# Kernel optimization log

Hardware: AMD Instinct MI355X
Metric: run time of the kernel (lower is better)

## Reference

```python
import jax, jax.numpy as jnp
import numpy as np

B, C_IN, H, W = 8, 112, 16, 16
D = 128            # patch_embed_dim
N_BANK = 200000
CHUNK = 1024       # query_chunk_size
NN_K = 3
TOPK_RATIO = 0.03  # reduction = 'topk_mean'


def setup_inputs() -> dict:
    key = jax.random.key(0)
    k1, k2, k3 = jax.random.split(key, 3)
    feature_map = jax.random.normal(k1, (B, C_IN, H, W), dtype=jnp.float32)
    proj_w = jax.random.normal(k2, (D, C_IN), dtype=jnp.float32) * 0.05
    memory_bank = jax.random.normal(k3, (N_BANK, D), dtype=jnp.float32)
    return {"feature_map": feature_map, "proj_w": proj_w, "memory_bank": memory_bank}


def _l2norm(x, axis=-1, eps=1e-12):
    return x / jnp.maximum(jnp.linalg.norm(x, axis=axis, keepdims=True), eps)


def reference(feature_map, proj_w, memory_bank):
    b, c, h, w = feature_map.shape
    patches = h * w
    # patch embeddings: NHWC flatten -> linear proj (no bias) -> L2 normalize
    emb = feature_map.transpose(0, 2, 3, 1).reshape(-1, c)        # [Q, C_in]
    emb = _l2norm(emb @ proj_w.T)                                  # [Q, D]
    bank = _l2norm(memory_bank)                                    # [N, D]
    bank_t = bank.T                                                # [D, N]

    q_total = emb.shape[0]
    n_chunks = q_total // CHUNK if q_total % CHUNK == 0 else -(-q_total // CHUNK)
    pad = n_chunks * CHUNK - q_total
    emb_p = jnp.pad(emb, ((0, pad), (0, 0)))
    chunks = emb_p.reshape(n_chunks, CHUNK, -1)

    def chunk_fn(q):                                               # q: [CHUNK, D]
        sims = q @ bank_t                                          # [CHUNK, N]
        best_sim, _ = jax.lax.top_k(sims, NN_K)                    # [CHUNK, k]
        dist = jnp.sqrt(jnp.maximum(2.0 - 2.0 * best_sim, 0.0))
        return dist.mean(axis=1)                                   # [CHUNK]

    patch_d = jax.lax.map(chunk_fn, chunks).reshape(-1)[:q_total]
    patch_d = patch_d.reshape(b, patches)                          # [B, P]

    # topk_mean reduction over patches
    k = min(patches, max(1, int(np.ceil(patches * TOPK_RATIO))))
    top_vals, _ = jax.lax.top_k(patch_d, k)
    return top_vals.mean(axis=1)                                   # [B]
```

## Files before the change

### kernel.cpp

```cpp
#include <hip/hip_runtime.h>
#include <stdint.h>

#define N_BANK 200000
#define N_PAD  201600
#define NQ     2048
#define DIMD   128
#define C_IN   112
#define NCHUNK 63
#define CHUNK_COLS 3200
#define STEP_COLS 64
#define NSTEP  50
#define NCE    126
#define NC3    378

typedef short v8s __attribute__((ext_vector_type(8)));
typedef float v4f __attribute__((ext_vector_type(4)));

typedef const __attribute__((address_space(1))) uint32_t* gp1_t;
typedef __attribute__((address_space(3))) uint32_t* lp3_t;

__device__ __forceinline__ void async16(const void* g, void* l) {
  __builtin_amdgcn_global_load_lds((gp1_t)g, (lp3_t)l, 16, 0, 0);
}

__device__ __forceinline__ unsigned short f2bf(float f) {
  uint32_t u = __float_as_uint(f);
  u += 0x7fff + ((u >> 16) & 1);
  return (unsigned short)(u >> 16);
}

__device__ __forceinline__ void insert3(float& m1, float& m2, float& m3, float v) {
  m3 = __builtin_amdgcn_fmed3f(m2, m3, v);
  m2 = __builtin_amdgcn_fmed3f(m1, m2, v);
  m1 = fmaxf(m1, v);
}

__global__ void emb_kernel(const float* __restrict__ fm, const float* __restrict__ pw,
                           unsigned short* __restrict__ embB) {
  int q = blockIdx.x;
  int b = q >> 8, p = q & 255;
  int tid = threadIdx.x;
  __shared__ float x[C_IN];
  __shared__ float wsum[2];
  if (tid < C_IN) x[tid] = fm[(b * C_IN + tid) * 256 + p];
  __syncthreads();
  const float* row = pw + tid * C_IN;
  float dot = 0.f;
#pragma unroll
  for (int c = 0; c < C_IN; ++c) dot = fmaf(x[c], row[c], dot);
  float s = dot * dot;
#pragma unroll
  for (int off = 32; off; off >>= 1) s += __shfl_xor(s, off);
  int lane = tid & 63, wv = tid >> 6;
  if (lane == 0) wsum[wv] = s;
  __syncthreads();
  float ss = wsum[0] + wsum[1];
  float scale = 1.f / fmaxf(sqrtf(ss), 1e-12f);
  int j = tid >> 3, pos = tid & 7;
  int sw = j ^ (q & 15);
  embB[q * DIMD + sw * 8 + pos] = f2bf(dot * scale);
}

__global__ void bank_kernel(const float* __restrict__ bank, unsigned short* __restrict__ bankB) {
  int tid = threadIdx.x;
  int wv = tid >> 6, lane = tid & 63;
  int r = blockIdx.x * 4 + wv;
  if (r >= N_PAD) return;
  uint32_t* out = (uint32_t*)bankB;
  int j = lane >> 2, w = lane & 3;
  int sdw = ((j ^ (r & 15)) << 2) | w;
  if (r < N_BANK) {
    float2 v = ((const float2*)bank)[r * 64 + lane];
    float s = v.x * v.x + v.y * v.y;
#pragma unroll
    for (int off = 32; off; off >>= 1) s += __shfl_xor(s, off);
    float scale = 1.f / fmaxf(sqrtf(s), 1e-12f);
    uint32_t lo = f2bf(v.x * scale);
    uint32_t hi = f2bf(v.y * scale);
    out[r * 64 + sdw] = lo | (hi << 16);
  } else {
    out[r * 64 + sdw] = 0u;
  }
}

__global__ __launch_bounds__(256, 2)
void sim_top3_kernel(const unsigned short* __restrict__ embB,
                     const unsigned short* __restrict__ bankB,
                     float* __restrict__ partial) {
  int id = blockIdx.x;
  int chunk, mt;
  if (id < 896) {
    int x = id & 7, j = id >> 3;
    chunk = x * 7 + (j >> 4);
    mt = j & 15;
  } else {
    int t2 = id - 896;
    chunk = 56 + (t2 >> 4);
    mt = t2 & 15;
  }
  int q0 = mt * 128;
  int tid = threadIdx.x;
  int wv = tid >> 6, lane = tid & 63;
  int wr = wv >> 1, wc = wv & 1;
  int g = lane >> 4, c0 = lane & 15;

  __shared__ __align__(16) unsigned char lds[32768];

  {
    const char* gbase = (const char*)embB + q0 * 256;
#pragma unroll
    for (int i = 0; i < 8; ++i) {
      int off = i * 4096 + tid * 16;
      async16(gbase + off, lds + off);
    }
  }
  asm volatile("s_waitcnt vmcnt(0)" ::: "memory");
  __builtin_amdgcn_sched_barrier(0);
  __builtin_amdgcn_s_barrier();

  v8s a[4][4];
#pragma unroll
  for (int fm = 0; fm < 4; ++fm)
#pragma unroll
    for (int k = 0; k < 4; ++k) {
      int row = wr * 64 + fm * 16 + c0;
      a[fm][k] = *(const v8s*)(lds + row * 256 + (((k * 4 + g) ^ c0) << 4));
    }
  asm volatile("s_waitcnt lgkmcnt(0)" ::: "memory");
  __builtin_amdgcn_sched_barrier(0);
  __builtin_amdgcn_s_barrier();

  float m1[16], m2[16], m3[16];
#pragma unroll
  for (int t = 0; t < 16; ++t) { m1[t] = -1e30f; m2[t] = -1e30f; m3[t] = -1e30f; }

  const char* bbase = (const char*)bankB + (size_t)chunk * CHUNK_COLS * 256;

#pragma unroll
  for (int i = 0; i < 4; ++i) {
    int off = i * 4096 + tid * 16;
    async16(bbase + off, lds + off);
  }

  for (int s = 0; s < NSTEP; ++s) {
    if (s + 1 < NSTEP) {
      const char* gsrc = bbase + (size_t)(s + 1) * (STEP_COLS * 256);
      unsigned char* ldst = lds + ((s + 1) & 1) * 16384;
#pragma unroll
      for (int i = 0; i < 4; ++i) {
        int off = i * 4096 + tid * 16;
        async16(gsrc + off, ldst + off);
      }
      asm volatile("s_waitcnt vmcnt(4)" ::: "memory");
    } else {
      asm volatile("s_waitcnt vmcnt(0)" ::: "memory");
    }
    __builtin_amdgcn_sched_barrier(0);
    __builtin_amdgcn_s_barrier();

    const unsigned char* bp = lds + (s & 1) * 16384;
#pragma unroll
    for (int fn = 0; fn < 2; ++fn) {
      v8s bf[4];
      int col = wc * 32 + fn * 16 + c0;
#pragma unroll
      for (int k = 0; k < 4; ++k)
        bf[k] = *(const v8s*)(bp + col * 256 + (((k * 4 + g) ^ c0) << 4));
#pragma unroll
      for (int fm = 0; fm < 4; ++fm) {
        v4f acc = {0.f, 0.f, 0.f, 0.f};
#pragma unroll
        for (int k = 0; k < 4; ++k)
          acc = __builtin_amdgcn_mfma_f32_16x16x32_bf16(a[fm][k], bf[k], acc, 0, 0, 0);
#pragma unroll
        for (int j = 0; j < 4; ++j)
          insert3(m1[fm * 4 + j], m2[fm * 4 + j], m3[fm * 4 + j], acc[j]);
      }
    }
    __builtin_amdgcn_s_barrier();
  }

#pragma unroll
  for (int mask = 1; mask < 16; mask <<= 1) {
#pragma unroll
    for (int t = 0; t < 16; ++t) {
      float b1 = __shfl_xor(m1[t], mask);
      float b2 = __shfl_xor(m2[t], mask);
      float b3 = __shfl_xor(m3[t], mask);
      insert3(m1[t], m2[t], m3[t], b1);
      insert3(m1[t], m2[t], m3[t], b2);
      insert3(m1[t], m2[t], m3[t], b3);
    }
  }

  if (c0 == 0) {
    int ce = chunk * 2 + wc;
#pragma unroll
    for (int t = 0; t < 16; ++t) {
      int q = q0 + wr * 64 + (t >> 2) * 16 + g * 4 + (t & 3);
      float* dst = partial + (size_t)q * NC3 + ce * 3;
      dst[0] = m1[t];
      dst[1] = m2[t];
      dst[2] = m3[t];
    }
  }
}

__global__ void merge1_kernel(const float* __restrict__ partial, float* __restrict__ pd) {
  int q = (blockIdx.x * blockDim.x + threadIdx.x) >> 6;
  int lane = threadIdx.x & 63;
  const float* src = partial + (size_t)q * NC3;
  float m1 = -1e30f, m2 = -1e30f, m3 = -1e30f;
  for (int c = lane; c < NC3; c += 64) insert3(m1, m2, m3, src[c]);
#pragma unroll
  for (int mask = 32; mask; mask >>= 1) {
    float b1 = __shfl_xor(m1, mask);
    float b2 = __shfl_xor(m2, mask);
    float b3 = __shfl_xor(m3, mask);
    insert3(m1, m2, m3, b1);
    insert3(m1, m2, m3, b2);
    insert3(m1, m2, m3, b3);
  }
  if (lane == 0) {
    float d1 = sqrtf(fmaxf(2.f - 2.f * m1, 0.f));
    float d2 = sqrtf(fmaxf(2.f - 2.f * m2, 0.f));
    float d3 = sqrtf(fmaxf(2.f - 2.f * m3, 0.f));
    pd[q] = (d1 + d2 + d3) * (1.f / 3.f);
  }
}

__global__ void merge2_kernel(const float* __restrict__ pd, float* __restrict__ out) {
  int b = blockIdx.x;
  int tid = threadIdx.x;
  __shared__ float vals[256];
  __shared__ float rv[256];
  __shared__ int ri[256];
  vals[tid] = pd[b * 256 + tid];
  __syncthreads();
  float sum = 0.f;
  for (int iter = 0; iter < 8; ++iter) {
    rv[tid] = vals[tid]; ri[tid] = tid;
    __syncthreads();
    for (int s = 128; s > 0; s >>= 1) {
      if (tid < s && rv[tid + s] > rv[tid]) { rv[tid] = rv[tid + s]; ri[tid] = ri[tid + s]; }
      __syncthreads();
    }
    sum += rv[0];
    if (tid == 0) vals[ri[0]] = -1e30f;
    __syncthreads();
  }
  if (tid == 0) out[b] = sum * (1.f / 8.f);
}

extern "C" void kernel_launch(void* const* d_in, const int* in_sizes, int n_in,
                              void* d_out, int out_size, void* d_ws, size_t ws_size,
                              hipStream_t stream) {
  const float* fm   = (const float*)d_in[0];
  const float* pw   = (const float*)d_in[1];
  const float* bank = (const float*)d_in[2];
  float* out = (float*)d_out;

  char* ws = (char*)d_ws;
  unsigned short* bankB = (unsigned short*)ws;
  unsigned short* embB  = (unsigned short*)(ws + 51609600);
  float* partial        = (float*)(ws + 51609600 + 524288);
  float* pd             = (float*)(ws + 51609600 + 524288 + 3096576);

  emb_kernel<<<NQ, 128, 0, stream>>>(fm, pw, embB);
  bank_kernel<<<N_PAD / 4, 256, 0, stream>>>(bank, bankB);
  sim_top3_kernel<<<16 * NCHUNK, 256, 0, stream>>>(embB, bankB, partial);
  merge1_kernel<<<NQ / 4, 256, 0, stream>>>(partial, pd);
  merge2_kernel<<<8, 256, 0, stream>>>(pd, out);
}
```

Baseline: 310.7 us.

## Fuse prep kernels and merge kernels, raise sim kernel occupancy bound

Merges the embedding and bank normalization kernels into one launch, split by block index, and merges the two reduction kernels into a single final kernel. Launch_bounds for the similarity kernel goes from 2 to 4 waves per SIMD. The aim is fewer launches and more blocks resident per CU. The fused final kernel uses only 8 blocks with one thread per query reading 378 strided floats, so the merge becomes serial and poorly coalesced. The tighter occupancy bound may also force register spills in the sim kernel.

```diff
diff --git a/kernel.cpp b/kernel.cpp
--- a/kernel.cpp
+++ b/kernel.cpp
@@ -12,6 +12,8 @@
 #define NSTEP  50
 #define NCE    126
 #define NC3    378
+#define NBANKBLK 50400
+#define NEMBBLK  1024
 
 typedef short v8s __attribute__((ext_vector_type(8)));
 typedef float v4f __attribute__((ext_vector_type(4)));
@@ -35,55 +37,58 @@
   m1 = fmaxf(m1, v);
 }
 
-__global__ void emb_kernel(const float* __restrict__ fm, const float* __restrict__ pw,
-                           unsigned short* __restrict__ embB) {
-  int q = blockIdx.x;
-  int b = q >> 8, p = q & 255;
+__global__ void prep_kernel(const float* __restrict__ fm, const float* __restrict__ pw,
+                            const float* __restrict__ bank,
+                            unsigned short* __restrict__ embB,
+                            unsigned short* __restrict__ bankB) {
+  int blk = blockIdx.x;
   int tid = threadIdx.x;
-  __shared__ float x[C_IN];
-  __shared__ float wsum[2];
-  if (tid < C_IN) x[tid] = fm[(b * C_IN + tid) * 256 + p];
-  __syncthreads();
-  const float* row = pw + tid * C_IN;
-  float dot = 0.f;
-#pragma unroll
-  for (int c = 0; c < C_IN; ++c) dot = fmaf(x[c], row[c], dot);
-  float s = dot * dot;
-#pragma unroll
-  for (int off = 32; off; off >>= 1) s += __shfl_xor(s, off);
-  int lane = tid & 63, wv = tid >> 6;
-  if (lane == 0) wsum[wv] = s;
-  __syncthreads();
-  float ss = wsum[0] + wsum[1];
-  float scale = 1.f / fmaxf(sqrtf(ss), 1e-12f);
-  int j = tid >> 3, pos = tid & 7;
-  int sw = j ^ (q & 15);
-  embB[q * DIMD + sw * 8 + pos] = f2bf(dot * scale);
-}
-
-__global__ void bank_kernel(const float* __restrict__ bank, unsigned short* __restrict__ bankB) {
-  int tid = threadIdx.x;
-  int wv = tid >> 6, lane = tid & 63;
-  int r = blockIdx.x * 4 + wv;
-  if (r >= N_PAD) return;
-  uint32_t* out = (uint32_t*)bankB;
-  int j = lane >> 2, w = lane & 3;
-  int sdw = ((j ^ (r & 15)) << 2) | w;
-  if (r < N_BANK) {
-    float2 v = ((const float2*)bank)[r * 64 + lane];
-    float s = v.x * v.x + v.y * v.y;
+  if (blk < NBANKBLK) {
+    int wv = tid >> 6, lane = tid & 63;
+    int r = blk * 4 + wv;
+    uint32_t* out = (uint32_t*)bankB;
+    int j = lane >> 2, w = lane & 3;
+    int sdw = ((j ^ (r & 15)) << 2) | w;
+    if (r < N_BANK) {
+      float2 v = ((const float2*)bank)[r * 64 + lane];
+      float s = v.x * v.x + v.y * v.y;
+#pragma unroll
+      for (int off = 32; off; off >>= 1) s += __shfl_xor(s, off);
+      float scale = 1.f / fmaxf(sqrtf(s), 1e-12f);
+      uint32_t lo = f2bf(v.x * scale);
+      uint32_t hi = f2bf(v.y * scale);
+      out[r * 64 + sdw] = lo | (hi << 16);
+    } else {
+      out[r * 64 + sdw] = 0u;
+    }
+  } else {
+    __shared__ float x[2][C_IN];
+    __shared__ float wsum[4];
+    int half = tid >> 7;
+    int t = tid & 127;
+    int q = (blk - NBANKBLK) * 2 + half;
+    int b = q >> 8, p = q & 255;
+    if (t < C_IN) x[half][t] = fm[(b * C_IN + t) * 256 + p];
+    __syncthreads();
+    const float* row = pw + t * C_IN;
+    float dot = 0.f;
+#pragma unroll
+    for (int c = 0; c < C_IN; ++c) dot = fmaf(x[half][c], row[c], dot);
+    float s = dot * dot;
 #pragma unroll
     for (int off = 32; off; off >>= 1) s += __shfl_xor(s, off);
-    float scale = 1.f / fmaxf(sqrtf(s), 1e-12f);
-    uint32_t lo = f2bf(v.x * scale);
-    uint32_t hi = f2bf(v.y * scale);
-    out[r * 64 + sdw] = lo | (hi << 16);
-  } else {
-    out[r * 64 + sdw] = 0u;
-  }
-}
-
-__global__ __launch_bounds__(256, 2)
+    int wv = tid >> 6, lane = tid & 63;
+    if (lane == 0) wsum[wv] = s;
+    __syncthreads();
+    float ss = wsum[half * 2] + wsum[half * 2 + 1];
+    float scale = 1.f / fmaxf(sqrtf(ss), 1e-12f);
+    int j = t >> 3, pos = t & 7;
+    int sw = j ^ (q & 15);
+    embB[q * DIMD + sw * 8 + pos] = f2bf(dot * scale);
+  }
+}
+
+__global__ __launch_bounds__(256, 4)
 void sim_top3_kernel(const unsigned short* __restrict__ embB,
                      const unsigned short* __restrict__ bankB,
                      float* __restrict__ partial) {
@@ -206,36 +211,22 @@
   }
 }
 
-__global__ void merge1_kernel(const float* __restrict__ partial, float* __restrict__ pd) {
-  int q = (blockIdx.x * blockDim.x + threadIdx.x) >> 6;
-  int lane = threadIdx.x & 63;
+__global__ void final_kernel(const float* __restrict__ partial, float* __restrict__ out) {
+  int b = blockIdx.x;
+  int tid = threadIdx.x;
+  int q = b * 256 + tid;
   const float* src = partial + (size_t)q * NC3;
   float m1 = -1e30f, m2 = -1e30f, m3 = -1e30f;
-  for (int c = lane; c < NC3; c += 64) insert3(m1, m2, m3, src[c]);
-#pragma unroll
-  for (int mask = 32; mask; mask >>= 1) {
-    float b1 = __shfl_xor(m1, mask);
-    float b2 = __shfl_xor(m2, mask);
-    float b3 = __shfl_xor(m3, mask);
-    insert3(m1, m2, m3, b1);
-    insert3(m1, m2, m3, b2);
-    insert3(m1, m2, m3, b3);
-  }
-  if (lane == 0) {
-    float d1 = sqrtf(fmaxf(2.f - 2.f * m1, 0.f));
-    float d2 = sqrtf(fmaxf(2.f - 2.f * m2, 0.f));
-    float d3 = sqrtf(fmaxf(2.f - 2.f * m3, 0.f));
-    pd[q] = (d1 + d2 + d3) * (1.f / 3.f);
-  }
-}
-
-__global__ void merge2_kernel(const float* __restrict__ pd, float* __restrict__ out) {
-  int b = blockIdx.x;
-  int tid = threadIdx.x;
+  for (int c = 0; c < NC3; ++c) insert3(m1, m2, m3, src[c]);
+  float d1 = sqrtf(fmaxf(2.f - 2.f * m1, 0.f));
+  float d2 = sqrtf(fmaxf(2.f - 2.f * m2, 0.f));
+  float d3 = sqrtf(fmaxf(2.f - 2.f * m3, 0.f));
+  float d = (d1 + d2 + d3) * (1.f / 3.f);
+
   __shared__ float vals[256];
   __shared__ float rv[256];
   __shared__ int ri[256];
-  vals[tid] = pd[b * 256 + tid];
+  vals[tid] = d;
   __syncthreads();
   float sum = 0.f;
   for (int iter = 0; iter < 8; ++iter) {
@@ -264,11 +255,8 @@
   unsigned short* bankB = (unsigned short*)ws;
   unsigned short* embB  = (unsigned short*)(ws + 51609600);
   float* partial        = (float*)(ws + 51609600 + 524288);
-  float* pd             = (float*)(ws + 51609600 + 524288 + 3096576);
-
-  emb_kernel<<<NQ, 128, 0, stream>>>(fm, pw, embB);
-  bank_kernel<<<N_PAD / 4, 256, 0, stream>>>(bank, bankB);
+
+  prep_kernel<<<NBANKBLK + NEMBBLK, 256, 0, stream>>>(fm, pw, bank, embB, bankB);
   sim_top3_kernel<<<16 * NCHUNK, 256, 0, stream>>>(embB, bankB, partial);
-  merge1_kernel<<<NQ / 4, 256, 0, stream>>>(partial, pd);
-  merge2_kernel<<<8, 256, 0, stream>>>(pd, out);
-}
+  final_kernel<<<8, 256, 0, stream>>>(partial, out);
+}
```

Result: slower. 474.2 us (+52.6%).
